# Performance work log

Measured on AMD Instinct MI355X. Metric: run time of the kernel, lower is better.

Reference implementation:

```python
import jax, jax.numpy as jnp
import numpy as np

B, T, H, D, V = 1, 512, 12, 64, 32000  # batch, seq, heads, head_dim, vocab


def setup_inputs() -> dict:
    key = jax.random.key(0)
    k0, k1, k2, k3 = jax.random.split(key, 4)
    x = jax.random.normal(k0, (B, T, H * D), dtype=jnp.float32)
    # per-head FFN weights: torch Linear(head_dim, head_dim) -> weight (out,in)=(D,D)
    W_ffn = jax.random.normal(k1, (H, D, D), dtype=jnp.float32) * 0.02
    b_ffn = jnp.zeros((H, D), dtype=jnp.float32)
    # per-head vocab attention: torch Linear(head_dim, vocab_size, bias=False) -> weight (V,D)
    W_vocab = jax.random.normal(k2, (H, V, D), dtype=jnp.float32) * 0.02
    temps = jnp.ones((H,), dtype=jnp.float32)
    # shared vocab embedding table (vocab_size, n_embd)
    E = jax.random.normal(k3, (V, H * D), dtype=jnp.float32) * 0.02
    return {"x": x, "W_ffn": W_ffn, "b_ffn": b_ffn, "W_vocab": W_vocab,
            "temps": temps, "E": E}


def reference(x, W_ffn, b_ffn, W_vocab, temps, E):
    Bx, Tx, C = x.shape
    Hn, Dn, _ = W_ffn.shape
    xh = x.reshape(Bx, Tx, Hn, Dn)                         # (B,T,H,D)
    # per-head FFN (Linear: y = x @ W^T + b)
    ffn = jnp.einsum('bthd,hed->bthe', xh, W_ffn) + b_ffn  # (B,T,H,D)
    # per-head vocab logits against weight bank (H,V,D)
    logits = jnp.einsum('bthd,hvd->bthv', ffn, W_vocab)    # (B,T,H,V)
    temp = jnp.maximum(temps, 0.1)[None, None, :, None]    # clamp(min=0.1)
    w = jax.nn.softmax(logits / temp, axis=-1)             # (B,T,H,V)
    # back-project through per-head slices of vocab embedding table
    Eh = E.reshape(E.shape[0], Hn, Dn)                     # (V,H,D)
    out = jnp.einsum('bthv,vhd->bthd', w, Eh)              # (B,T,H,D)
    # dropout is identity at eval (p used at train only)
    return out.reshape(Bx, Tx, C)
```

## Files before the change

### kernel.cpp

```cpp
#include <hip/hip_runtime.h>
#include <hip/hip_bf16.h>
#include <cstddef>

#define T_TOK 512
#define NH    12
#define HD    64
#define NV    32000
#define CEMB  768
#define NC    50
#define VC    (NV/NC)
#define NSUB  (VC/64)
#define QTILE 256
#define LOG2E 1.44269504088896340736f

typedef short v8bf  __attribute__((ext_vector_type(8)));
typedef float v16f  __attribute__((ext_vector_type(16)));
typedef unsigned uv4 __attribute__((ext_vector_type(4)));

__device__ __forceinline__ unsigned short f2bf(float f) {
    unsigned u = __float_as_uint(f);
    u += 0x7fffu + ((u >> 16) & 1u);
    return (unsigned short)(u >> 16);
}
__device__ __forceinline__ unsigned cvtpk(float a, float b) {
    unsigned r;
    asm("v_cvt_pk_bf16_f32 %0, %1, %2" : "=v"(r) : "v"(a), "v"(b));
    return r;
}
__device__ __forceinline__ void pl32swap(unsigned &x, unsigned &y) {
    asm("v_permlane32_swap_b32 %0, %1" : "+v"(x), "+v"(y));
}
__device__ __forceinline__ float bf2f(unsigned short u) {
    return __uint_as_float(((unsigned)u) << 16);
}
__device__ __forceinline__ void gld16(const void* g, void* l) {
    __builtin_amdgcn_global_load_lds(
        (const __attribute__((address_space(1))) unsigned*)g,
        (__attribute__((address_space(3))) unsigned*)l, 16, 0, 0);
}

__global__ __launch_bounds__(256) void ffn_kernel(
        const float* __restrict__ x, const float* __restrict__ Wf,
        const float* __restrict__ bf, const float* __restrict__ temps,
        unsigned short* __restrict__ Qb) {
    const int h = blockIdx.y;
    const int tl = threadIdx.x >> 6, e = threadIdx.x & 63;
    const int t = blockIdx.x * 4 + tl;
    __shared__ float xs[4][HD];
    xs[tl][e] = x[t*CEMB + h*HD + e];
    __syncthreads();
    const float4* w4  = (const float4*)(Wf + (size_t)(h*HD + e)*HD);
    const float4* xs4 = (const float4*)xs[tl];
    float acc = bf[h*HD + e];
    #pragma unroll
    for (int i = 0; i < HD/4; ++i) {
        float4 a = xs4[i], b = w4[i];
        acc += a.x*b.x + a.y*b.y + a.z*b.z + a.w*b.w;
    }
    float tau = temps[h]; tau = (tau < 0.1f) ? 0.1f : tau;
    Qb[((size_t)h*T_TOK + t)*HD + e] = f2bf(acc * LOG2E / tau);
}

__global__ __launch_bounds__(256) void e_transpose(const float* __restrict__ E,
                                                   unsigned short* __restrict__ ET) {
    const int v0 = blockIdx.x * 64, h = blockIdx.y;
    const int tid = threadIdx.x;
    __shared__ float Ts[64*65];
    #pragma unroll
    for (int r = 0; r < 4; ++r) {
        int f = tid + 256*r, v = f >> 4, d4 = f & 15;
        float4 e4 = *(const float4*)&E[(size_t)(v0 + v)*CEMB + h*HD + d4*4];
        Ts[(d4*4+0)*65 + v] = e4.x;
        Ts[(d4*4+1)*65 + v] = e4.y;
        Ts[(d4*4+2)*65 + v] = e4.z;
        Ts[(d4*4+3)*65 + v] = e4.w;
    }
    __syncthreads();
    #pragma unroll
    for (int r = 0; r < 2; ++r) {
        int u = tid + 256*r, d = u >> 3, c16 = u & 7;
        const float* row = &Ts[d*65 + c16*8];
        uint4 w;
        w.x = cvtpk(row[0], row[1]);
        w.y = cvtpk(row[2], row[3]);
        w.z = cvtpk(row[4], row[5]);
        w.w = cvtpk(row[6], row[7]);
        *(uint4*)&ET[(size_t)(h*64 + d)*NV + v0 + c16*8] = w;
    }
}

__global__ __launch_bounds__(512, 4) void flash_mfma(
        const unsigned short* __restrict__ Qb, const float* __restrict__ Wv,
        const unsigned short* __restrict__ ET, unsigned short* __restrict__ Npart,
        float* __restrict__ Zpart) {
    const int g    = blockIdx.x;
    const int xcd  = g & 7, slot = g >> 3;
    const int qg   = slot & 1;
    const int p    = (slot >> 1)*8 + xcd;
    const int c    = p % NC;
    const int h    = p / NC;

    const int tid  = threadIdx.x;
    const int wq   = tid >> 6;
    const int lane = tid & 63;
    const int l31  = lane & 31, hi = lane >> 5;

    __shared__ unsigned short Kb[2][64*64];
    __shared__ unsigned short Eb[2][64*64];

    const int tbase = qg*QTILE + wq*32;

    v8bf qf[4];
    #pragma unroll
    for (int k16 = 0; k16 < 4; ++k16)
        qf[k16] = *(const v8bf*)&Qb[((size_t)h*T_TOK + tbase + l31)*HD
                                    + k16*16 + hi*8];

    v16f o0, o1;
    #pragma unroll
    for (int r = 0; r < 16; ++r) { o0[r] = 0.f; o1[r] = 0.f; }
    float zacc = 0.f;

    const int kv = wq*8 + (lane >> 3);
    const float* kgl = Wv + ((size_t)h*NV + (size_t)c*VC + kv)*HD + (lane & 7)*8;
    const int kwoff = kv*64 + (((lane & 7) ^ (lane >> 3)))*8;
    const unsigned short* eg = ET + (size_t)(h*64 + wq*8 + (lane >> 3))*NV
                                  + (size_t)c*VC + (((lane & 7) ^ (lane >> 3)))*8;

    {
        gld16(eg, &Eb[0][(wq*8)*64]);
        float4 a = *(const float4*)(kgl);
        float4 b = *(const float4*)(kgl + 4);
        uv4 w = { cvtpk(a.x,a.y), cvtpk(a.z,a.w), cvtpk(b.x,b.y), cvtpk(b.z,b.w) };
        *(uv4*)&Kb[0][kwoff] = w;
        __syncthreads();
    }

    int nb = 1;
    for (int s = 0; s < NSUB; ++s) {
        const int cur = nb ^ 1;
        const bool pre = (s + 1 < NSUB);
        float4 ka, kb2;
        if (pre) {
            gld16(eg + (s+1)*64, &Eb[nb][(wq*8)*64]);
            ka  = *(const float4*)(kgl + (size_t)(s+1)*4096);
            kb2 = *(const float4*)(kgl + (size_t)(s+1)*4096 + 4);
        }

        uv4 pfw[4];
        #pragma unroll
        for (int vt = 0; vt < 2; ++vt) {
            v8bf kf[4];
            #pragma unroll
            for (int k16 = 0; k16 < 4; ++k16) {
                const int row = vt*32 + l31;
                kf[k16] = *(const v8bf*)&Kb[cur][row*64 + ((k16*2 + hi) ^ (row & 7))*8];
            }
            v16f sa;
            #pragma unroll
            for (int r = 0; r < 16; ++r) sa[r] = 0.f;
            #pragma unroll
            for (int k16 = 0; k16 < 4; ++k16)
                sa = __builtin_amdgcn_mfma_f32_32x32x16_bf16(kf[k16], qf[k16], sa, 0, 0, 0);
            unsigned W[8];
            #pragma unroll
            for (int gi = 0; gi < 4; ++gi) {
                float pa = __builtin_amdgcn_exp2f(sa[4*gi+0]);
                float pb = __builtin_amdgcn_exp2f(sa[4*gi+1]);
                float pc = __builtin_amdgcn_exp2f(sa[4*gi+2]);
                float pd = __builtin_amdgcn_exp2f(sa[4*gi+3]);
                zacc += (pa + pb) + (pc + pd);
                W[2*gi+0] = cvtpk(pa, pb);
                W[2*gi+1] = cvtpk(pc, pd);
            }
            unsigned x0 = W[0], y0 = W[2];  pl32swap(x0, y0);
            unsigned x1 = W[1], y1 = W[3];  pl32swap(x1, y1);
            pfw[vt*2 + 0] = (uv4){ x0, x1, y0, y1 };
            unsigned x2 = W[4], y2 = W[6];  pl32swap(x2, y2);
            unsigned x3 = W[5], y3 = W[7];  pl32swap(x3, y3);
            pfw[vt*2 + 1] = (uv4){ x2, x3, y2, y3 };
        }

        #pragma unroll
        for (int dt = 0; dt < 2; ++dt) {
            v8bf ef[4];
            #pragma unroll
            for (int k16 = 0; k16 < 4; ++k16) {
                const int row = dt*32 + l31;
                ef[k16] = *(const v8bf*)&Eb[cur][row*64 + ((k16*2 + hi) ^ (row & 7))*8];
            }
            v16f oo = dt ? o1 : o0;
            #pragma unroll
            for (int k16 = 0; k16 < 4; ++k16)
                oo = __builtin_amdgcn_mfma_f32_32x32x16_bf16(
                        ef[k16], __builtin_bit_cast(v8bf, pfw[k16]), oo, 0, 0, 0);
            if (dt) o1 = oo; else o0 = oo;
        }

        if (pre) {
            uv4 w = { cvtpk(ka.x,ka.y), cvtpk(ka.z,ka.w),
                      cvtpk(kb2.x,kb2.y), cvtpk(kb2.z,kb2.w) };
            *(uv4*)&Kb[nb][kwoff] = w;
            __syncthreads();
        }
        nb ^= 1;
    }

    zacc += __shfl_xor(zacc, 32, 64);
    if (hi == 0)
        Zpart[((size_t)c*T_TOK + tbase + l31)*NH + h] = zacc;

    {
        const int t = tbase + l31;
        unsigned short* np = Npart + (((size_t)c*T_TOK + t)*NH + h)*HD;
        #pragma unroll
        for (int dt = 0; dt < 2; ++dt) {
            v16f oo = dt ? o1 : o0;
            #pragma unroll
            for (int gi = 0; gi < 4; ++gi) {
                uint2 w = { cvtpk(oo[4*gi+0], oo[4*gi+1]),
                            cvtpk(oo[4*gi+2], oo[4*gi+3]) };
                *(uint2*)&np[dt*32 + gi*8 + hi*4] = w;
            }
        }
    }
}

__global__ void combine_kernel(const unsigned short* __restrict__ Npart,
                               const float* __restrict__ Zpart,
                               float* __restrict__ out) {
    const int idx = (blockIdx.x*256 + threadIdx.x)*4;
    const int t = idx / CEMB;
    const int rem = idx % CEMB;
    const int h = rem >> 6, d = rem & 63;
    float n0 = 0.f, n1 = 0.f, n2 = 0.f, n3 = 0.f, z = 0.f;
    #pragma unroll
    for (int c = 0; c < NC; ++c) {
        uint2 u = *(const uint2*)&Npart[(((size_t)c*T_TOK + t)*NH + h)*HD + d];
        n0 += bf2f((unsigned short)(u.x & 0xffffu));
        n1 += bf2f((unsigned short)(u.x >> 16));
        n2 += bf2f((unsigned short)(u.y & 0xffffu));
        n3 += bf2f((unsigned short)(u.y >> 16));
        z  += Zpart[((size_t)c*T_TOK + t)*NH + h];
    }
    const float rz = 1.0f / z;
    float4 o = { n0*rz, n1*rz, n2*rz, n3*rz };
    *(float4*)&out[idx] = o;
}

extern "C" void kernel_launch(void* const* d_in, const int* in_sizes, int n_in,
                              void* d_out, int out_size, void* d_ws, size_t ws_size,
                              hipStream_t stream) {
    const float* x     = (const float*)d_in[0];
    const float* Wf    = (const float*)d_in[1];
    const float* bf    = (const float*)d_in[2];
    const float* Wv    = (const float*)d_in[3];
    const float* temps = (const float*)d_in[4];
    const float* E     = (const float*)d_in[5];
    float* out = (float*)d_out;

    char* ws = (char*)d_ws;
    unsigned short* Npart = (unsigned short*)ws;
    float*          Zpart = (float*)(ws + 39321600);
    unsigned short* Qb    = (unsigned short*)(ws + 40550400);
    unsigned short* ET    = (unsigned short*)(ws + 41336832);

    e_transpose   <<<dim3(NV/64, NH),         256, 0, stream>>>(E, ET);
    ffn_kernel    <<<dim3(T_TOK/4, NH),       256, 0, stream>>>(x, Wf, bf, temps, Qb);
    flash_mfma    <<<dim3(NC*2*NH),           512, 0, stream>>>(Qb, Wv, ET, Npart, Zpart);
    combine_kernel<<<dim3((T_TOK*CEMB)/1024), 256, 0, stream>>>(Npart, Zpart, out);
}
```

Measured before the change: 302.3 us.

## Process all 512 queries per block with 1024 threads and split K/E loading across waves

```diff
diff --git a/kernel.cpp b/kernel.cpp
--- a/kernel.cpp
+++ b/kernel.cpp
@@ -10,7 +10,6 @@
 #define NC    50
 #define VC    (NV/NC)
 #define NSUB  (VC/64)
-#define QTILE 256
 #define LOG2E 1.44269504088896340736f
 
 typedef short v8bf  __attribute__((ext_vector_type(8)));
@@ -89,16 +88,12 @@
     }
 }
 
-__global__ __launch_bounds__(512, 4) void flash_mfma(
+__global__ __launch_bounds__(1024, 2) void flash_mfma(
         const unsigned short* __restrict__ Qb, const float* __restrict__ Wv,
         const unsigned short* __restrict__ ET, unsigned short* __restrict__ Npart,
         float* __restrict__ Zpart) {
-    const int g    = blockIdx.x;
-    const int xcd  = g & 7, slot = g >> 3;
-    const int qg   = slot & 1;
-    const int p    = (slot >> 1)*8 + xcd;
-    const int c    = p % NC;
-    const int h    = p / NC;
+    const int c = blockIdx.x % NC;
+    const int h = blockIdx.x / NC;
 
     const int tid  = threadIdx.x;
     const int wq   = tid >> 6;
@@ -108,7 +103,7 @@
     __shared__ unsigned short Kb[2][64*64];
     __shared__ unsigned short Eb[2][64*64];
 
-    const int tbase = qg*QTILE + wq*32;
+    const int tbase = wq*32;
 
     v8bf qf[4];
     #pragma unroll
@@ -121,20 +116,23 @@
     for (int r = 0; r < 16; ++r) { o0[r] = 0.f; o1[r] = 0.f; }
     float zacc = 0.f;
 
-    const int kv = wq*8 + (lane >> 3);
+    const int wr   = wq & 7;
+    const bool isE = (wq < 8);
+    const int kv = wr*8 + (lane >> 3);
     const float* kgl = Wv + ((size_t)h*NV + (size_t)c*VC + kv)*HD + (lane & 7)*8;
     const int kwoff = kv*64 + (((lane & 7) ^ (lane >> 3)))*8;
-    const unsigned short* eg = ET + (size_t)(h*64 + wq*8 + (lane >> 3))*NV
+    const unsigned short* eg = ET + (size_t)(h*64 + wr*8 + (lane >> 3))*NV
                                   + (size_t)c*VC + (((lane & 7) ^ (lane >> 3)))*8;
 
-    {
-        gld16(eg, &Eb[0][(wq*8)*64]);
+    if (isE) {
+        gld16(eg, &Eb[0][(wr*8)*64]);
+    } else {
         float4 a = *(const float4*)(kgl);
         float4 b = *(const float4*)(kgl + 4);
         uv4 w = { cvtpk(a.x,a.y), cvtpk(a.z,a.w), cvtpk(b.x,b.y), cvtpk(b.z,b.w) };
         *(uv4*)&Kb[0][kwoff] = w;
-        __syncthreads();
-    }
+    }
+    __syncthreads();
 
     int nb = 1;
     for (int s = 0; s < NSUB; ++s) {
@@ -142,9 +140,12 @@
         const bool pre = (s + 1 < NSUB);
         float4 ka, kb2;
         if (pre) {
-            gld16(eg + (s+1)*64, &Eb[nb][(wq*8)*64]);
-            ka  = *(const float4*)(kgl + (size_t)(s+1)*4096);
-            kb2 = *(const float4*)(kgl + (size_t)(s+1)*4096 + 4);
+            if (isE) {
+                gld16(eg + (s+1)*64, &Eb[nb][(wr*8)*64]);
+            } else {
+                ka  = *(const float4*)(kgl + (size_t)(s+1)*4096);
+                kb2 = *(const float4*)(kgl + (size_t)(s+1)*4096 + 4);
+            }
         }
 
         uv4 pfw[4];
@@ -159,9 +160,11 @@
             v16f sa;
             #pragma unroll
             for (int r = 0; r < 16; ++r) sa[r] = 0.f;
+            __builtin_amdgcn_s_setprio(1);
             #pragma unroll
             for (int k16 = 0; k16 < 4; ++k16)
                 sa = __builtin_amdgcn_mfma_f32_32x32x16_bf16(kf[k16], qf[k16], sa, 0, 0, 0);
+            __builtin_amdgcn_s_setprio(0);
             unsigned W[8];
             #pragma unroll
             for (int gi = 0; gi < 4; ++gi) {
@@ -181,6 +184,12 @@
             pfw[vt*2 + 1] = (uv4){ x2, x3, y2, y3 };
         }
 
+        if (pre && !isE) {
+            uv4 w = { cvtpk(ka.x,ka.y), cvtpk(ka.z,ka.w),
+                      cvtpk(kb2.x,kb2.y), cvtpk(kb2.z,kb2.w) };
+            *(uv4*)&Kb[nb][kwoff] = w;
+        }
+
         #pragma unroll
         for (int dt = 0; dt < 2; ++dt) {
             v8bf ef[4];
@@ -190,19 +199,16 @@
                 ef[k16] = *(const v8bf*)&Eb[cur][row*64 + ((k16*2 + hi) ^ (row & 7))*8];
             }
             v16f oo = dt ? o1 : o0;
+            __builtin_amdgcn_s_setprio(1);
             #pragma unroll
             for (int k16 = 0; k16 < 4; ++k16)
                 oo = __builtin_amdgcn_mfma_f32_32x32x16_bf16(
                         ef[k16], __builtin_bit_cast(v8bf, pfw[k16]), oo, 0, 0, 0);
+            __builtin_amdgcn_s_setprio(0);
             if (dt) o1 = oo; else o0 = oo;
         }
 
-        if (pre) {
-            uv4 w = { cvtpk(ka.x,ka.y), cvtpk(ka.z,ka.w),
-                      cvtpk(kb2.x,kb2.y), cvtpk(kb2.z,kb2.w) };
-            *(uv4*)&Kb[nb][kwoff] = w;
-            __syncthreads();
-        }
+        if (pre) __syncthreads();
         nb ^= 1;
     }
 
@@ -267,6 +273,6 @@
 
     e_transpose   <<<dim3(NV/64, NH),         256, 0, stream>>>(E, ET);
     ffn_kernel    <<<dim3(T_TOK/4, NH),       256, 0, stream>>>(x, Wf, bf, temps, Qb);
-    flash_mfma    <<<dim3(NC*2*NH),           512, 0, stream>>>(Qb, Wv, ET, Npart, Zpart);
+    flash_mfma    <<<dim3(NC*NH),            1024, 0, stream>>>(Qb, Wv, ET, Npart, Zpart);
     combine_kernel<<<dim3((T_TOK*CEMB)/1024), 256, 0, stream>>>(Npart, Zpart, out);
 }
```

Measured after the change: 305.6 us. No clear change (+1.1%).
